# Performance work log

Hardware: AMD Instinct MI355X
Metric: run time of the kernel (lower is better)

The kernel has to match this reference:

```python
import jax, jax.numpy as jnp
import numpy as np

DIM = 256
NUM_HEADS = 8
AGENT_NUM = 49
POOL = 7  # int(sqrt(agent_num))


def setup_inputs() -> dict:
    key = jax.random.key(0)
    k1, k2, k3, k4, k5 = jax.random.split(key, 5)
    x = jax.random.normal(k1, (8, 8, 8, 14, 14, DIM), dtype=jnp.float32)
    wq = jax.random.normal(k2, (DIM, DIM), dtype=jnp.float32) * 0.02
    wkv = jax.random.normal(k3, (2 * DIM, DIM), dtype=jnp.float32) * 0.02
    w_proj = jax.random.normal(k4, (DIM, DIM), dtype=jnp.float32) * 0.02
    b_proj = jax.random.normal(k5, (DIM,), dtype=jnp.float32) * 0.02
    return {"x": x, "wq": wq, "wkv": wkv, "w_proj": w_proj, "b_proj": b_proj}


def reference(x, wq, wkv, w_proj, b_proj):
    B, Hh, Ww, wh, ww, c = x.shape
    b = B * Hh * Ww
    n = wh * ww
    H, W = ww, wh  # module uses (H, W) = (window_width, window_height)
    nh = NUM_HEADS
    hd = c // nh
    scale = hd ** -0.5

    xt = x.reshape(b, n, c)  # (b x y)(w1 w2) d
    q = xt @ wq.T                          # [b, n, c]
    kv = xt @ wkv.T                        # [b, n, 2c]
    k, v = kv[..., :c], kv[..., c:]

    # agent tokens: adaptive avg pool q over the window grid to POOL x POOL
    qs = q.reshape(b, H, W, c)
    agent = qs.reshape(b, POOL, H // POOL, POOL, W // POOL, c).mean(axis=(2, 4))
    agent = agent.reshape(b, AGENT_NUM, c)

    # split heads -> [b, nh, seq, hd]
    qh = q.reshape(b, n, nh, hd).transpose(0, 2, 1, 3)
    kh = k.reshape(b, n, nh, hd).transpose(0, 2, 1, 3)
    vh = v.reshape(b, n, nh, hd).transpose(0, 2, 1, 3)
    ah = agent.reshape(b, AGENT_NUM, nh, hd).transpose(0, 2, 1, 3)

    # stage 1: agents attend over k/v
    agent_attn = jax.nn.softmax(jnp.einsum('bhad,bhnd->bhan', ah * scale, kh), axis=-1)
    agent_v = jnp.einsum('bhan,bhnd->bhad', agent_attn, vh)

    # stage 2: queries attend over agents
    q_attn = jax.nn.softmax(jnp.einsum('bhnd,bhad->bhna', qh * scale, ah), axis=-1)
    out = jnp.einsum('bhna,bhad->bhnd', q_attn, agent_v)

    out = out.transpose(0, 2, 1, 3).reshape(b, n, c)
    out = out @ w_proj.T + b_proj
    # rearrange '(b x y) (i j) c -> b x y i j c' with i = window_width
    return out.reshape(B, Hh, Ww, ww, wh, c)
```

## Files before the change

kernel.cpp:

```cpp
#include <hip/hip_runtime.h>

typedef unsigned short u16;
typedef __attribute__((ext_vector_type(8))) short bf16x8;
typedef __attribute__((ext_vector_type(4))) float f32x4;

#define M_ROWS 100352
#define NB     512
#define NTOK   196
#define CDIM   256
#define NHEADS 8
#define HDIM   32
#define ANUM   49

__device__ __forceinline__ u16 f2bf(float f) {
    union { float f; unsigned u; } c; c.f = f;
    return (u16)((c.u + 0x7FFFu + ((c.u >> 16) & 1u)) >> 16);
}
__device__ __forceinline__ float bf2f(u16 u) {
    union { unsigned u; float f; } c; c.u = ((unsigned)u) << 16;
    return c.f;
}

#define NX4 6422528
__global__ __launch_bounds__(256)
void cast_all(const float* __restrict__ x, const float* __restrict__ wq,
              const float* __restrict__ wkv, const float* __restrict__ wproj,
              u16* __restrict__ xb, u16* __restrict__ wqkvb,
              u16* __restrict__ wprojb)
{
    const int idx4 = blockIdx.x * 256 + threadIdx.x;
    const float* src; u16* dst; int off;
    if (idx4 < NX4)               { src = x;     dst = xb;             off = idx4; }
    else if (idx4 < NX4 + 16384)  { src = wq;    dst = wqkvb;          off = idx4 - NX4; }
    else if (idx4 < NX4 + 49152)  { src = wkv;   dst = wqkvb + 65536;  off = idx4 - NX4 - 16384; }
    else                          { src = wproj; dst = wprojb;         off = idx4 - NX4 - 49152; }
    float4 v = *reinterpret_cast<const float4*>(&src[(size_t)off * 4]);
    ushort4 o;
    o.x = f2bf(v.x); o.y = f2bf(v.y); o.z = f2bf(v.z); o.w = f2bf(v.w);
    *reinterpret_cast<ushort4*>(&dst[(size_t)off * 4]) = o;
}

#define GLD 40
__global__ __launch_bounds__(256)
void gemm_qkv(const u16* __restrict__ xb, const u16* __restrict__ wqkvb,
              u16* __restrict__ qb, u16* __restrict__ kvb)
{
    __shared__ u16 As[128 * GLD];
    __shared__ u16 Bs[128 * GLD];

    const int tid  = threadIdx.x;
    const int lane = tid & 63, wid = tid >> 6;
    const int wm = wid >> 1, wn = wid & 1;
    const int row0 = blockIdx.x * 128;
    const int col0 = blockIdx.y * 128;

    f32x4 acc[4][4] = {};
    const int lrow = lane & 15;
    const int lk   = (lane >> 4) * 8;

    for (int k0 = 0; k0 < 256; k0 += 32) {
        #pragma unroll
        for (int i = 0; i < 2; ++i) {
            const int c = tid + i * 256;
            const int r = c >> 2, kc = c & 3;
            bf16x8 va = *reinterpret_cast<const bf16x8*>(
                &xb[(size_t)(row0 + r) * 256 + k0 + kc * 8]);
            *reinterpret_cast<bf16x8*>(&As[r * GLD + kc * 8]) = va;
            bf16x8 vb = *reinterpret_cast<const bf16x8*>(
                &wqkvb[(size_t)(col0 + r) * 256 + k0 + kc * 8]);
            *reinterpret_cast<bf16x8*>(&Bs[r * GLD + kc * 8]) = vb;
        }
        __syncthreads();

        bf16x8 af[4], bfr[4];
        #pragma unroll
        for (int m = 0; m < 4; ++m)
            af[m] = *reinterpret_cast<bf16x8*>(&As[(wm*64 + m*16 + lrow) * GLD + lk]);
        #pragma unroll
        for (int n = 0; n < 4; ++n)
            bfr[n] = *reinterpret_cast<bf16x8*>(&Bs[(wn*64 + n*16 + lrow) * GLD + lk]);
        #pragma unroll
        for (int m = 0; m < 4; ++m)
            #pragma unroll
            for (int n = 0; n < 4; ++n)
                acc[m][n] = __builtin_amdgcn_mfma_f32_16x16x32_bf16(
                                af[m], bfr[n], acc[m][n], 0, 0, 0);
        __syncthreads();
    }

    const bool isq = (col0 < 256);
    u16* C = isq ? qb : kvb;
    const int ldc = isq ? 256 : 512;
    const int cb  = isq ? col0 : col0 - 256;
    #pragma unroll
    for (int n = 0; n < 4; ++n) {
        const int ccol = cb + wn*64 + n*16 + (lane & 15);
        #pragma unroll
        for (int m = 0; m < 4; ++m) {
            const int rbase = row0 + wm*64 + m*16 + (lane >> 4) * 4;
            #pragma unroll
            for (int r = 0; r < 4; ++r)
                C[(size_t)(rbase + r) * ldc + ccol] = f2bf(acc[m][n][r]);
        }
    }
}

__global__ __launch_bounds__(256)
void gemm_proj(const u16* __restrict__ A, const u16* __restrict__ Bw,
               const float* __restrict__ bias, float* __restrict__ C)
{
    __shared__ u16 As[128 * GLD];
    __shared__ u16 Bs[128 * GLD];

    const int tid  = threadIdx.x;
    const int lane = tid & 63, wid = tid >> 6;
    const int wm = wid >> 1, wn = wid & 1;
    const int row0 = blockIdx.x * 128;
    const int col0 = blockIdx.y * 128;

    f32x4 acc[4][4] = {};
    const int lrow = lane & 15;
    const int lk   = (lane >> 4) * 8;

    for (int k0 = 0; k0 < 256; k0 += 32) {
        #pragma unroll
        for (int i = 0; i < 2; ++i) {
            const int c = tid + i * 256;
            const int r = c >> 2, kc = c & 3;
            bf16x8 va = *reinterpret_cast<const bf16x8*>(
                &A[(size_t)(row0 + r) * 256 + k0 + kc * 8]);
            *reinterpret_cast<bf16x8*>(&As[r * GLD + kc * 8]) = va;
            bf16x8 vb = *reinterpret_cast<const bf16x8*>(
                &Bw[(size_t)(col0 + r) * 256 + k0 + kc * 8]);
            *reinterpret_cast<bf16x8*>(&Bs[r * GLD + kc * 8]) = vb;
        }
        __syncthreads();

        bf16x8 af[4], bfr[4];
        #pragma unroll
        for (int m = 0; m < 4; ++m)
            af[m] = *reinterpret_cast<bf16x8*>(&As[(wm*64 + m*16 + lrow) * GLD + lk]);
        #pragma unroll
        for (int n = 0; n < 4; ++n)
            bfr[n] = *reinterpret_cast<bf16x8*>(&Bs[(wn*64 + n*16 + lrow) * GLD + lk]);
        #pragma unroll
        for (int m = 0; m < 4; ++m)
            #pragma unroll
            for (int n = 0; n < 4; ++n)
                acc[m][n] = __builtin_amdgcn_mfma_f32_16x16x32_bf16(
                                af[m], bfr[n], acc[m][n], 0, 0, 0);
        __syncthreads();
    }

    #pragma unroll
    for (int n = 0; n < 4; ++n) {
        const int ccol = col0 + wn*64 + n*16 + (lane & 15);
        const float bv = bias[ccol];
        #pragma unroll
        for (int m = 0; m < 4; ++m) {
            const int rbase = row0 + wm*64 + m*16 + (lane >> 4) * 4;
            #pragma unroll
            for (int r = 0; r < 4; ++r)
                C[(size_t)(rbase + r) * 256 + ccol] = acc[m][n][r] + bv;
        }
    }
}

__global__ __launch_bounds__(256)
void pool_kernel(const u16* __restrict__ qb, u16* __restrict__ agentb)
{
    const int idx = blockIdx.x * 256 + threadIdx.x;
    const int ch = idx & 255;
    const int a  = (idx >> 8) % ANUM;
    const int b  = idx / (ANUM * CDIM);
    const int p1 = a / 7, p2 = a % 7;
    const u16* q0 = qb + (size_t)b * NTOK * CDIM;
    float s = 0.f;
    #pragma unroll
    for (int i2 = 0; i2 < 2; ++i2)
        #pragma unroll
        for (int j2 = 0; j2 < 2; ++j2) {
            const int n = (p1*2 + i2) * 14 + (p2*2 + j2);
            s += bf2f(q0[(size_t)n * CDIM + ch]);
        }
    agentb[idx] = f2bf(0.25f * s);
}

#define SA_LD   40
#define SK_LD   40
#define SVT_LD  232
#define SP1_LD  232
#define SAVT_LD 72
#define SP2_LD  72
#define OFF_A   0
#define OFF_K   2560
#define OFF_VT  10880
#define OFF_P2  2560
#define OFF_P1  18304
#define OFF_AVT 33152
#define LDS_U16 35456

__global__ __launch_bounds__(256)
void fused_attn(const u16* __restrict__ kvb, const u16* __restrict__ agentb,
                u16* __restrict__ qb)
{
    __shared__ __align__(16) u16 lds[LDS_U16];
    const int tid  = threadIdx.x;
    const int lane = tid & 63, w = tid >> 6;
    const int li = lane & 15, g = lane >> 4;
    const int b = blockIdx.x >> 3, h = blockIdx.x & 7;
    const float scale = 0.1767766952966369f;
    const f32x4 z = {0.f, 0.f, 0.f, 0.f};

    for (int i = tid; i < LDS_U16 / 8; i += 256)
        *reinterpret_cast<f32x4*>(&lds[i * 8]) = z;
    __syncthreads();

    {
        const int a = tid >> 2, kc = tid & 3;
        if (a < ANUM) {
            bf16x8 v = *reinterpret_cast<const bf16x8*>(
                &agentb[((size_t)b * ANUM + a) * CDIM + h * HDIM + kc * 8]);
            bf16x8 t;
            #pragma unroll
            for (int j2 = 0; j2 < 8; ++j2)
                t[j2] = (short)f2bf(bf2f((u16)v[j2]) * scale);
            *reinterpret_cast<bf16x8*>(&lds[OFF_A + a * SA_LD + kc * 8]) = t;
        }
    }
    for (int i = tid; i < NTOK * 4; i += 256) {
        const int n = i >> 2, kc = i & 3;
        bf16x8 v = *reinterpret_cast<const bf16x8*>(
            &kvb[((size_t)(b * NTOK + n)) * 512 + h * HDIM + kc * 8]);
        *reinterpret_cast<bf16x8*>(&lds[OFF_K + n * SK_LD + kc * 8]) = v;
    }
    for (int i = tid; i < NTOK * 2; i += 256) {
        const int n = i >> 1, dh = i & 1;
        const u16* src = &kvb[((size_t)(b * NTOK + n)) * 512 + 256 + h * HDIM + dh * 16];
        bf16x8 v0 = *reinterpret_cast<const bf16x8*>(src);
        bf16x8 v1 = *reinterpret_cast<const bf16x8*>(src + 8);
        #pragma unroll
        for (int j2 = 0; j2 < 8; ++j2) {
            lds[OFF_VT + (dh * 16 + j2) * SVT_LD + n]     = (u16)v0[j2];
            lds[OFF_VT + (dh * 16 + 8 + j2) * SVT_LD + n] = (u16)v1[j2];
        }
    }
    __syncthreads();

    {
        bf16x8 af = *reinterpret_cast<bf16x8*>(&lds[OFF_A + (w*16 + li) * SA_LD + g*8]);
        f32x4 c[13];
        #pragma unroll
        for (int j = 0; j < 13; ++j) {
            bf16x8 kf = *reinterpret_cast<bf16x8*>(&lds[OFF_K + (j*16 + li) * SK_LD + g*8]);
            c[j] = __builtin_amdgcn_mfma_f32_16x16x32_bf16(af, kf, z, 0, 0, 0);
        }
        #pragma unroll
        for (int r = 0; r < 4; ++r) {
            float m = -1e30f;
            #pragma unroll
            for (int j = 0; j < 13; ++j)
                if (j < 12 || li < 4) m = fmaxf(m, c[j][r]);
            #pragma unroll
            for (int d = 1; d < 16; d <<= 1) m = fmaxf(m, __shfl_xor(m, d));
            float p[13]; float su = 0.f;
            #pragma unroll
            for (int j = 0; j < 13; ++j) {
                p[j] = (j < 12 || li < 4) ? __expf(c[j][r] - m) : 0.f;
                su += p[j];
            }
            #pragma unroll
            for (int d = 1; d < 16; d <<= 1) su += __shfl_xor(su, d);
            const float inv = 1.f / su;
            const int arow = w*16 + g*4 + r;
            #pragma unroll
            for (int j = 0; j < 13; ++j)
                lds[OFF_P1 + arow * SP1_LD + j*16 + li] = f2bf(p[j] * inv);
        }
    }
    __syncthreads();

    #pragma unroll
    for (int dt = 0; dt < 2; ++dt) {
        f32x4 acc = z;
        #pragma unroll
        for (int kk = 0; kk < 7; ++kk) {
            bf16x8 pa = *reinterpret_cast<bf16x8*>(
                &lds[OFF_P1 + (w*16 + li) * SP1_LD + kk*32 + g*8]);
            bf16x8 vb = *reinterpret_cast<bf16x8*>(
                &lds[OFF_VT + (dt*16 + li) * SVT_LD + kk*32 + g*8]);
            acc = __builtin_amdgcn_mfma_f32_16x16x32_bf16(pa, vb, acc, 0, 0, 0);
        }
        #pragma unroll
        for (int r = 0; r < 4; ++r)
            lds[OFF_AVT + (dt*16 + li) * SAVT_LD + w*16 + g*4 + r] = f2bf(acc[r]);
    }
    __syncthreads();

    {
        bf16x8 ab[4];
        #pragma unroll
        for (int at = 0; at < 4; ++at)
            ab[at] = *reinterpret_cast<bf16x8*>(&lds[OFF_A + (at*16 + li) * SA_LD + g*8]);
        for (int j = w; j < 13; j += 4) {
            const int qrow = min(j*16 + li, NTOK - 1);
            bf16x8 qf = *reinterpret_cast<const bf16x8*>(
                &qb[((size_t)(b * NTOK) + qrow) * CDIM + h * HDIM + g*8]);
            f32x4 cc[4];
            #pragma unroll
            for (int at = 0; at < 4; ++at)
                cc[at] = __builtin_amdgcn_mfma_f32_16x16x32_bf16(qf, ab[at], z, 0, 0, 0);
            #pragma unroll
            for (int r = 0; r < 4; ++r) {
                float m = -1e30f;
                #pragma unroll
                for (int at = 0; at < 4; ++at)
                    if (at < 3 || li < 1) m = fmaxf(m, cc[at][r]);
                #pragma unroll
                for (int d = 1; d < 16; d <<= 1) m = fmaxf(m, __shfl_xor(m, d));
                float p[4]; float su = 0.f;
                #pragma unroll
                for (int at = 0; at < 4; ++at) {
                    p[at] = (at < 3 || li < 1) ? __expf(cc[at][r] - m) : 0.f;
                    su += p[at];
                }
                #pragma unroll
                for (int d = 1; d < 16; d <<= 1) su += __shfl_xor(su, d);
                const float inv = 1.f / su;
                const int trow = j*16 + g*4 + r;
                #pragma unroll
                for (int at = 0; at < 4; ++at)
                    lds[OFF_P2 + trow * SP2_LD + at*16 + li] = f2bf(p[at] * inv);
            }
        }
    }
    __syncthreads();

    for (int j = w; j < 13; j += 4) {
        #pragma unroll
        for (int dt = 0; dt < 2; ++dt) {
            f32x4 acc = z;
            #pragma unroll
            for (int kk = 0; kk < 2; ++kk) {
                bf16x8 pf = *reinterpret_cast<bf16x8*>(
                    &lds[OFF_P2 + (j*16 + li) * SP2_LD + kk*32 + g*8]);
                bf16x8 avf = *reinterpret_cast<bf16x8*>(
                    &lds[OFF_AVT + (dt*16 + li) * SAVT_LD + kk*32 + g*8]);
                acc = __builtin_amdgcn_mfma_f32_16x16x32_bf16(pf, avf, acc, 0, 0, 0);
            }
            #pragma unroll
            for (int r = 0; r < 4; ++r) {
                const int t = j*16 + g*4 + r;
                if (t < NTOK)
                    qb[((size_t)(b * NTOK) + t) * CDIM + h * HDIM + dt*16 + li]
                        = f2bf(acc[r]);
            }
        }
    }
}

extern "C" void kernel_launch(void* const* d_in, const int* in_sizes, int n_in,
                              void* d_out, int out_size, void* d_ws, size_t ws_size,
                              hipStream_t stream)
{
    const float* x     = (const float*)d_in[0];
    const float* wq    = (const float*)d_in[1];
    const float* wkv   = (const float*)d_in[2];
    const float* wproj = (const float*)d_in[3];
    const float* bproj = (const float*)d_in[4];
    float* out = (float*)d_out;

    u16* wqkvb  = (u16*)d_ws;
    u16* wprojb = wqkvb  + 196608;
    u16* xb     = wprojb + 65536;
    u16* qb     = xb     + (size_t)M_ROWS * CDIM;
    u16* agentb = qb     + (size_t)M_ROWS * CDIM;
    u16* kvb    = agentb + (size_t)NB*ANUM*CDIM;

    const dim3 blk(256);

    cast_all<<<dim3(25344), blk, 0, stream>>>(x, wq, wkv, wproj, xb, wqkvb, wprojb);
    gemm_qkv<<<dim3(M_ROWS/128, 6), blk, 0, stream>>>(xb, wqkvb, qb, kvb);
    pool_kernel<<<dim3((NB*ANUM*CDIM)/256), blk, 0, stream>>>(qb, agentb);
    fused_attn<<<dim3(NB*NHEADS), blk, 0, stream>>>(kvb, agentb, qb);
    gemm_proj<<<dim3(M_ROWS/128, 2), blk, 0, stream>>>(qb, wprojb, bproj, out);
}
```

Before: 454.7 us.

## Fuse agent pooling into attention kernel and read K directly from global

Removes the separate pool kernel and computes the 2x2-averaged, pre-scaled agent tokens inside the attention block from this head's q slice. K fragments are now loaded straight from global memory into MFMA operands instead of being staged in LDS, with row indices clamped for padding. Only the padded regions of LDS are zeroed instead of the whole buffer. The LDS footprint shrinks and launch bounds now request 3 blocks per CU for higher occupancy. The cost is uncoalesced global K reads and possible extra cache traffic.

```diff
diff --git a/kernel.cpp b/kernel.cpp
--- a/kernel.cpp
+++ b/kernel.cpp
@@ -166,43 +166,20 @@
     }
 }
 
-__global__ __launch_bounds__(256)
-void pool_kernel(const u16* __restrict__ qb, u16* __restrict__ agentb)
-{
-    const int idx = blockIdx.x * 256 + threadIdx.x;
-    const int ch = idx & 255;
-    const int a  = (idx >> 8) % ANUM;
-    const int b  = idx / (ANUM * CDIM);
-    const int p1 = a / 7, p2 = a % 7;
-    const u16* q0 = qb + (size_t)b * NTOK * CDIM;
-    float s = 0.f;
-    #pragma unroll
-    for (int i2 = 0; i2 < 2; ++i2)
-        #pragma unroll
-        for (int j2 = 0; j2 < 2; ++j2) {
-            const int n = (p1*2 + i2) * 14 + (p2*2 + j2);
-            s += bf2f(q0[(size_t)n * CDIM + ch]);
-        }
-    agentb[idx] = f2bf(0.25f * s);
-}
-
 #define SA_LD   40
-#define SK_LD   40
 #define SVT_LD  232
 #define SP1_LD  232
 #define SAVT_LD 72
 #define SP2_LD  72
 #define OFF_A   0
-#define OFF_K   2560
-#define OFF_VT  10880
+#define OFF_VT  2560
+#define OFF_P1  9984
+#define OFF_AVT 24832
 #define OFF_P2  2560
-#define OFF_P1  18304
-#define OFF_AVT 33152
-#define LDS_U16 35456
-
-__global__ __launch_bounds__(256)
-void fused_attn(const u16* __restrict__ kvb, const u16* __restrict__ agentb,
-                u16* __restrict__ qb)
+#define LDS_U16 27136
+
+__global__ __launch_bounds__(256, 3)
+void fused_attn(const u16* __restrict__ kvb, u16* __restrict__ qb)
 {
     __shared__ __align__(16) u16 lds[LDS_U16];
     const int tid  = threadIdx.x;
@@ -211,29 +188,44 @@
     const int b = blockIdx.x >> 3, h = blockIdx.x & 7;
     const float scale = 0.1767766952966369f;
     const f32x4 z = {0.f, 0.f, 0.f, 0.f};
-
-    for (int i = tid; i < LDS_U16 / 8; i += 256)
-        *reinterpret_cast<f32x4*>(&lds[i * 8]) = z;
-    __syncthreads();
-
-    {
-        const int a = tid >> 2, kc = tid & 3;
-        if (a < ANUM) {
-            bf16x8 v = *reinterpret_cast<const bf16x8*>(
-                &agentb[((size_t)b * ANUM + a) * CDIM + h * HDIM + kc * 8]);
-            bf16x8 t;
-            #pragma unroll
-            for (int j2 = 0; j2 < 8; ++j2)
-                t[j2] = (short)f2bf(bf2f((u16)v[j2]) * scale);
-            *reinterpret_cast<bf16x8*>(&lds[OFF_A + a * SA_LD + kc * 8]) = t;
-        }
-    }
-    for (int i = tid; i < NTOK * 4; i += 256) {
-        const int n = i >> 2, kc = i & 3;
-        bf16x8 v = *reinterpret_cast<const bf16x8*>(
-            &kvb[((size_t)(b * NTOK + n)) * 512 + h * HDIM + kc * 8]);
-        *reinterpret_cast<bf16x8*>(&lds[OFF_K + n * SK_LD + kc * 8]) = v;
-    }
+    const bf16x8 zv = {0,0,0,0,0,0,0,0};
+    const ushort4 z4 = {0,0,0,0};
+
+    for (int i = tid; i < 60; i += 256) {
+        const int row = 49 + (i >> 2), kc = i & 3;
+        *reinterpret_cast<bf16x8*>(&lds[OFF_A + row * SA_LD + kc * 8]) = zv;
+    }
+    for (int i = tid; i < 224; i += 256) {
+        const int row = i / 7, c4 = 196 + (i % 7) * 4;
+        *reinterpret_cast<ushort4*>(&lds[OFF_VT + row * SVT_LD + c4]) = z4;
+    }
+    for (int i = tid; i < 128; i += 256) {
+        const int row = i >> 1, c = 208 + (i & 1) * 8;
+        *reinterpret_cast<bf16x8*>(&lds[OFF_P1 + row * SP1_LD + c]) = zv;
+    }
+
+    const u16* qslice = qb + (size_t)b * NTOK * CDIM + h * HDIM;
+    for (int i = tid; i < ANUM * 8; i += 256) {
+        const int a = i >> 3, dq = (i & 7) * 4;
+        const int p1 = a / 7, p2 = a - p1 * 7;
+        float s0 = 0.f, s1 = 0.f, s2 = 0.f, s3 = 0.f;
+        #pragma unroll
+        for (int i2 = 0; i2 < 2; ++i2)
+            #pragma unroll
+            for (int j2 = 0; j2 < 2; ++j2) {
+                const int n = (p1*2 + i2) * 14 + p2*2 + j2;
+                ushort4 v = *reinterpret_cast<const ushort4*>(
+                    &qslice[(size_t)n * CDIM + dq]);
+                s0 += bf2f(v.x); s1 += bf2f(v.y);
+                s2 += bf2f(v.z); s3 += bf2f(v.w);
+            }
+        const float cc = 0.25f * scale;
+        ushort4 o;
+        o.x = f2bf(s0 * cc); o.y = f2bf(s1 * cc);
+        o.z = f2bf(s2 * cc); o.w = f2bf(s3 * cc);
+        *reinterpret_cast<ushort4*>(&lds[OFF_A + a * SA_LD + dq]) = o;
+    }
+
     for (int i = tid; i < NTOK * 2; i += 256) {
         const int n = i >> 1, dh = i & 1;
         const u16* src = &kvb[((size_t)(b * NTOK + n)) * 512 + 256 + h * HDIM + dh * 16];
@@ -252,7 +244,9 @@
         f32x4 c[13];
         #pragma unroll
         for (int j = 0; j < 13; ++j) {
-            bf16x8 kf = *reinterpret_cast<bf16x8*>(&lds[OFF_K + (j*16 + li) * SK_LD + g*8]);
+            int krow = j*16 + li; krow = krow > 195 ? 195 : krow;
+            bf16x8 kf = *reinterpret_cast<const bf16x8*>(
+                &kvb[((size_t)(b * NTOK + krow)) * 512 + h * HDIM + g*8]);
             c[j] = __builtin_amdgcn_mfma_f32_16x16x32_bf16(af, kf, z, 0, 0, 0);
         }
         #pragma unroll
@@ -374,14 +368,12 @@
     u16* wprojb = wqkvb  + 196608;
     u16* xb     = wprojb + 65536;
     u16* qb     = xb     + (size_t)M_ROWS * CDIM;
-    u16* agentb = qb     + (size_t)M_ROWS * CDIM;
-    u16* kvb    = agentb + (size_t)NB*ANUM*CDIM;
+    u16* kvb    = qb     + (size_t)M_ROWS * CDIM;
 
     const dim3 blk(256);
 
     cast_all<<<dim3(25344), blk, 0, stream>>>(x, wq, wkv, wproj, xb, wqkvb, wprojb);
     gemm_qkv<<<dim3(M_ROWS/128, 6), blk, 0, stream>>>(xb, wqkvb, qb, kvb);
-    pool_kernel<<<dim3((NB*ANUM*CDIM)/256), blk, 0, stream>>>(qb, agentb);
-    fused_attn<<<dim3(NB*NHEADS), blk, 0, stream>>>(kvb, agentb, qb);
+    fused_attn<<<dim3(NB*NHEADS), blk, 0, stream>>>(kvb, qb);
     gemm_proj<<<dim3(M_ROWS/128, 2), blk, 0, stream>>>(qb, wprojb, bproj, out);
 }
```

Result: no change. 448.5 us (-1.4%).
